# Performance work log

Hardware: AMD Instinct MI355X
Metric: run time of the kernel (lower is better)

Reference implementation:

```python
import math
import jax, jax.numpy as jnp
import numpy as np

EMBED_DIM = 512
NUM_HEADS = 8
EDGE_VOC = 16
EDGE_PAD = 0
L, B = 512, 16


def setup_inputs() -> dict:
    key = jax.random.key(0)
    ks = jax.random.split(key, 8)
    x = jax.random.normal(ks[0], (L, B, EMBED_DIM), dtype=jnp.float32)
    edge = jax.random.randint(ks[1], (B, L, L), 0, EDGE_VOC, dtype=jnp.int32)
    key_padding_mask = jnp.zeros((B, L), dtype=bool)
    # causal additive mask, as from nn.Transformer.generate_square_subsequent_mask
    attn_mask = jnp.where(jnp.triu(jnp.ones((L, L), bool), k=1), -jnp.inf, 0.0).astype(jnp.float32)
    s = 1.0 / math.sqrt(EMBED_DIM)
    in_proj_w = jax.random.uniform(ks[2], (3 * EMBED_DIM, EMBED_DIM), jnp.float32, -s, s)
    in_proj_b = jnp.zeros((3 * EMBED_DIM,), jnp.float32)
    out_proj_w = jax.random.uniform(ks[3], (EMBED_DIM, EMBED_DIM), jnp.float32, -s, s)
    out_proj_b = jnp.zeros((EMBED_DIM,), jnp.float32)
    edge_emb = jax.random.normal(ks[4], (EDGE_VOC, NUM_HEADS), dtype=jnp.float32)
    edge_emb = edge_emb.at[EDGE_PAD].set(0.0)  # padding_idx row zeroed
    return {"x": x, "edge": edge, "key_padding_mask": key_padding_mask,
            "attn_mask": attn_mask, "in_proj_w": in_proj_w, "in_proj_b": in_proj_b,
            "out_proj_w": out_proj_w, "out_proj_b": out_proj_b, "edge_emb": edge_emb}


def reference(x, edge, key_padding_mask, attn_mask,
              in_proj_w, in_proj_b, out_proj_w, out_proj_b, edge_emb):
    length, bsz, embed_dim = x.shape
    H = edge_emb.shape[1]
    hd = embed_dim // H
    qkv = x @ in_proj_w.T + in_proj_b                       # (L, B, 3E)
    q, k, v = jnp.split(qkv, 3, axis=-1)
    # (L, B*H, hd) -> (B*H, L, hd)
    q = q.reshape(length, bsz * H, hd).transpose(1, 0, 2)
    k = k.reshape(length, bsz * H, hd).transpose(1, 0, 2)
    v = v.reshape(length, bsz * H, hd).transpose(1, 0, 2)
    # combine attn_mask with key padding
    mask = attn_mask[None]                                   # (1, L, L)
    kpm = jnp.broadcast_to(key_padding_mask[:, None, None, :],
                           (bsz, H, 1, length)).reshape(bsz * H, 1, length)
    mask = jnp.where(kpm, -jnp.inf, mask)                    # (B*H, 1/L, L)
    # edge bias: (B, L, L, H) -> (B*H, L, L)
    ebias = edge_emb[edge].transpose(0, 3, 1, 2).reshape(bsz * H, length, length)
    q = q / math.sqrt(hd)
    scores = jnp.einsum('bqd,bkd->bqk', q, k) + mask + ebias
    attn = jax.nn.softmax(scores, axis=-1)
    out = jnp.einsum('bqk,bkd->bqd', attn, v)                # (B*H, L, hd)
    out = out.transpose(1, 0, 2).reshape(length, bsz, embed_dim)
    return out @ out_proj_w.T + out_proj_b
```

## Files before the change

### kernel.cpp

```cpp
#include <hip/hip_runtime.h>
#include <hip/hip_bf16.h>


typedef __attribute__((ext_vector_type(8))) short bf16x8;
typedef __attribute__((ext_vector_type(4))) float f32x4;
typedef __attribute__((ext_vector_type(4))) int i32x4;

#define LOG2E 1.44269504088896340736f

__device__ inline void gll16(const void* g, const void* l) {
  __builtin_amdgcn_global_load_lds(
      (const __attribute__((address_space(1))) unsigned int*)g,
      (__attribute__((address_space(3))) unsigned int*)l, 16, 0, 0);
}

__device__ inline short f2bf(float x) {
  __hip_bfloat16 t = __float2bfloat16(x);
  return *reinterpret_cast<short*>(&t);
}

__device__ inline void cstore(__hip_bfloat16* C, size_t idx, float v) {
  C[idx] = __float2bfloat16(v);
}
__device__ inline void cstore(float* C, size_t idx, float v) { C[idx] = v; }

__global__ void cvt3(const float* __restrict__ x, const float* __restrict__ w1,
                     const float* __restrict__ w2, __hip_bfloat16* __restrict__ xb,
                     __hip_bfloat16* __restrict__ w1b,
                     __hip_bfloat16* __restrict__ w2b) {
  const int blk = blockIdx.x;
  const float* src;
  __hip_bfloat16* dst;
  int off;
  if (blk < 2048)      { src = x;  dst = xb;  off = blk; }
  else if (blk < 2432) { src = w1; dst = w1b; off = blk - 2048; }
  else                 { src = w2; dst = w2b; off = blk - 2432; }
  const int i = (off * 256 + threadIdx.x) * 8;
  const float4 a = *(const float4*)(src + i);
  const float4 b = *(const float4*)(src + i + 4);
  bf16x8 r;
  r[0] = f2bf(a.x); r[1] = f2bf(a.y); r[2] = f2bf(a.z); r[3] = f2bf(a.w);
  r[4] = f2bf(b.x); r[5] = f2bf(b.y); r[6] = f2bf(b.z); r[7] = f2bf(b.w);
  *(bf16x8*)(dst + i) = r;
}

template <int MT, int RB, typename TC>
__global__ __launch_bounds__(256, RB) void gemm_bt(
    const __hip_bfloat16* __restrict__ A,
    const __hip_bfloat16* __restrict__ W,
    const float* __restrict__ bias,
    TC* __restrict__ C, int N, int K) {
  constexpr int MI = MT / 32;
  __shared__ short As[MT * 32];
  __shared__ short Ws[128 * 32];
  const int tid = threadIdx.x;
  const int wave = tid >> 6, lane = tid & 63;
  const int c = lane & 15, quad = lane >> 4;
  const int nb = N >> 7;
  const int bx = blockIdx.x % nb, by = blockIdx.x / nb;
  const int m0 = by * MT, n0 = bx << 7;
  const int wm = wave >> 1, wn = wave & 1;

  f32x4 acc[MI][4] = {};
  const int ar = lane >> 2;
  const int ak = (lane & 3) * 8;

  for (int k0 = 0; k0 < K; k0 += 32) {
    __syncthreads();
#pragma unroll
    for (int i = 0; i < MT / 64; i++) {
      const int r0 = i * 64 + wave * 16;
      gll16(A + (size_t)(m0 + r0 + ar) * K + k0 + ak, &As[r0 * 32]);
    }
#pragma unroll
    for (int i = 0; i < 2; i++) {
      const int r0 = i * 64 + wave * 16;
      gll16(W + (size_t)(n0 + r0 + ar) * K + k0 + ak, &Ws[r0 * 32]);
    }
    __syncthreads();
    bf16x8 af[MI], bfr[4];
#pragma unroll
    for (int i = 0; i < MI; i++)
      af[i] = *(const bf16x8*)&As[(wm * (MT / 2) + i * 16 + c) * 32 + quad * 8];
#pragma unroll
    for (int j = 0; j < 4; j++)
      bfr[j] = *(const bf16x8*)&Ws[(wn * 64 + j * 16 + c) * 32 + quad * 8];
#pragma unroll
    for (int i = 0; i < MI; i++)
#pragma unroll
      for (int j = 0; j < 4; j++)
        acc[i][j] = __builtin_amdgcn_mfma_f32_16x16x32_bf16(af[i], bfr[j],
                                                            acc[i][j], 0, 0, 0);
  }
#pragma unroll
  for (int j = 0; j < 4; j++) {
    const int col = n0 + wn * 64 + j * 16 + c;
    const float bv = bias[col];
#pragma unroll
    for (int i = 0; i < MI; i++) {
      const int row = m0 + wm * (MT / 2) + i * 16 + quad * 4;
#pragma unroll
      for (int r = 0; r < 4; r++)
        cstore(C, (size_t)(row + r) * N + col, acc[i][j][r] + bv);
    }
  }
}

__global__ __launch_bounds__(256, 4) void attn_kernel(
    const __hip_bfloat16* __restrict__ qkv,
    const int* __restrict__ edge,
    const float* __restrict__ edge_emb,
    __hip_bfloat16* __restrict__ attn_out) {
  __shared__ short Ks[64 * 72];
  __shared__ short Vt[64 * 72];
  __shared__ short Ps[4][16 * 72];
  __shared__ float eeS[16];

  const int tid = threadIdx.x;
  const int wave = tid >> 6, lane = tid & 63;
  const int c = lane & 15, quad = lane >> 4;
  const int i = blockIdx.x;
  constexpr int pi[8] = {0, 7, 1, 6, 2, 5, 3, 4};
  const int xcd = i & 7;
  const int j = i >> 3;
  const int qb = pi[j & 7];
  const int h = (j >> 3) & 7;
  const int b = xcd + ((j >> 6) << 3);
  const int colq = h * 64;

  if (tid < 16) eeS[tid] = (edge_emb[tid * 8 + h] - 16.0f) * LOG2E;

  const int q_g = (qb << 6) + wave * 16 + c;
  bf16x8 qf0, qf1;
  {
    const __hip_bfloat16* qp_ = qkv + (size_t)(q_g * 16 + b) * 1536 + colq;
    qf0 = *(const bf16x8*)(qp_ + quad * 8);
    qf1 = *(const bf16x8*)(qp_ + 32 + quad * 8);
  }
  float lsum = 0.f;
  f32x4 o[4] = {};
  const int* erow = edge + ((size_t)(b * 512 + q_g)) * 512;

  const int r2 = tid >> 3;
  const int cc = (tid & 7) * 8;
  const int kcol0 = ((r2 << 1) & 7) | (((r2 >> 2) ^ (cc >> 3)) << 3);
  const size_t sbase0 = (size_t)((r2 * 2) * 16 + b) * 1536 + colq + cc;
  bf16x8 kreg[2], vreg[2];
  kreg[0] = *(const bf16x8*)(qkv + sbase0 + 512);
  vreg[0] = *(const bf16x8*)(qkv + sbase0 + 1024);
  kreg[1] = *(const bf16x8*)(qkv + sbase0 + 24576 + 512);
  vreg[1] = *(const bf16x8*)(qkv + sbase0 + 24576 + 1024);

  __syncthreads();

  const int nkt = qb + 1;
  for (int kt = 0; kt < nkt; kt++) {
    const int k0 = kt << 6;
    if (kt) __syncthreads();
    *(bf16x8*)&Ks[(r2 * 2) * 72 + cc] = kreg[0];
    *(bf16x8*)&Ks[(r2 * 2 + 1) * 72 + cc] = kreg[1];
#pragma unroll
    for (int j2 = 0; j2 < 8; j2++) {
      short2 p;
      p.x = vreg[0][j2];
      p.y = vreg[1][j2];
      *(short2*)&Vt[(cc + j2) * 72 + kcol0] = p;
    }
    if (kt + 1 < nkt) {
      const size_t nb_ = sbase0 + (size_t)(kt + 1) * 64 * 24576;
      kreg[0] = *(const bf16x8*)(qkv + nb_ + 512);
      vreg[0] = *(const bf16x8*)(qkv + nb_ + 1024);
      kreg[1] = *(const bf16x8*)(qkv + nb_ + 24576 + 512);
      vreg[1] = *(const bf16x8*)(qkv + nb_ + 24576 + 1024);
    }
    i32x4 e4[4];
#pragma unroll
    for (int mt = 0; mt < 4; mt++)
      e4[mt] = *(const i32x4*)(erow + k0 + mt * 16 + quad * 4);
    __syncthreads();

    f32x4 st[4];
#pragma unroll
    for (int mt = 0; mt < 4; mt++) {
      const bf16x8 ka = *(const bf16x8*)&Ks[(mt * 16 + c) * 72 + quad * 8];
      const bf16x8 kb = *(const bf16x8*)&Ks[(mt * 16 + c) * 72 + 32 + quad * 8];
      f32x4 z = {0.f, 0.f, 0.f, 0.f};
      z = __builtin_amdgcn_mfma_f32_16x16x32_bf16(ka, qf0, z, 0, 0, 0);
      st[mt] = __builtin_amdgcn_mfma_f32_16x16x32_bf16(kb, qf1, z, 0, 0, 0);
    }
    float rsum = 0.0f;
#pragma unroll
    for (int mt = 0; mt < 4; mt++) {
      short4 pk;
#pragma unroll
      for (int r = 0; r < 4; r++) {
        const int key = k0 + mt * 16 + quad * 4 + r;
        const float p = (key <= q_g)
            ? exp2f(fmaf(st[mt][r], 0.125f * LOG2E, eeS[e4[mt][r] & 15]))
            : 0.0f;
        rsum += p;
        ((short*)&pk)[r] = f2bf(p);
      }
      *(short4*)&Ps[wave][c * 72 + mt * 16 + quad * 4] = pk;
    }
    lsum += rsum;
    const bf16x8 pa0 = *(const bf16x8*)&Ps[wave][c * 72 + quad * 8];
    const bf16x8 pa1 = *(const bf16x8*)&Ps[wave][c * 72 + 32 + quad * 8];
#pragma unroll
    for (int nt = 0; nt < 4; nt++) {
      const int n = nt * 16 + c;
      const bf16x8 vb0 = *(const bf16x8*)&Vt[n * 72 + ((quad ^ (n >> 3)) << 3)];
      const bf16x8 vb1 =
          *(const bf16x8*)&Vt[n * 72 + (((4 + quad) ^ (n >> 3)) << 3)];
      o[nt] = __builtin_amdgcn_mfma_f32_16x16x32_bf16(pa0, vb0, o[nt], 0, 0, 0);
      o[nt] = __builtin_amdgcn_mfma_f32_16x16x32_bf16(pa1, vb1, o[nt], 0, 0, 0);
    }
  }

  float l = lsum;
  l += __shfl_xor(l, 16);
  l += __shfl_xor(l, 32);
  float lr[4];
#pragma unroll
  for (int r = 0; r < 4; r++) lr[r] = __shfl(l, quad * 4 + r, 16);
  const int qrow0 = (qb << 6) + wave * 16 + quad * 4;
#pragma unroll
  for (int nt = 0; nt < 4; nt++)
#pragma unroll
    for (int r = 0; r < 4; r++)
      attn_out[(size_t)((qrow0 + r) * 16 + b) * 512 + colq + nt * 16 + c] =
          __float2bfloat16(o[nt][r] / lr[r]);
}

extern "C" void kernel_launch(void* const* d_in, const int* in_sizes, int n_in,
                              void* d_out, int out_size, void* d_ws, size_t ws_size,
                              hipStream_t stream) {
  const float* x    = (const float*)d_in[0];
  const int* edge   = (const int*)d_in[1];
  const float* ipw  = (const float*)d_in[4];
  const float* ipb  = (const float*)d_in[5];
  const float* opw  = (const float*)d_in[6];
  const float* opb  = (const float*)d_in[7];
  const float* eemb = (const float*)d_in[8];
  float* out = (float*)d_out;

  __hip_bfloat16* qkv  = (__hip_bfloat16*)d_ws;
  __hip_bfloat16* attn = qkv + (size_t)8192 * 1536;
  __hip_bfloat16* xb   = attn + (size_t)8192 * 512;
  __hip_bfloat16* w1b  = xb + (size_t)8192 * 512;
  __hip_bfloat16* w2b  = w1b + (size_t)1536 * 512;

  cvt3<<<2560, 256, 0, stream>>>(x, ipw, opw, xb, w1b, w2b);
  gemm_bt<128, 3, __hip_bfloat16>
      <<<768, 256, 0, stream>>>(xb, w1b, ipb, qkv, 1536, 512);
  attn_kernel<<<1024, 256, 0, stream>>>(qkv, edge, eemb, attn);
  gemm_bt<64, 2, float>
      <<<512, 256, 0, stream>>>(attn, w2b, opb, out, 512, 512);
}
```

Measured before the change: 155.6 us.

## Skip masked causal tiles on diagonal, fold QK scale into projection, seed MFMA with bias

On the diagonal key tile, each wave now computes only the 16-key sub-tiles at or below its query rows and skips the upper half of the PV MFMAs when they are all masked. The softmax scale times log2e is folded into the Q columns of the QKV projection epilogue. The edge bias is loaded as the MFMA accumulator seed, which removes the per-element fma. s_setprio hints are placed around the MFMA sections. Together these cut wasted causal work and VALU instructions in the attention inner loop, at the cost of more branches and storing Q pre-scaled in bf16, which changes rounding slightly. The bias lookup also relies on eeS being pre-scaled by log2e in code not shown, and the edge & 15 guard is dropped.

```diff
diff --git a/kernel.cpp b/kernel.cpp
--- a/kernel.cpp
+++ b/kernel.cpp
@@ -7,6 +7,7 @@
 typedef __attribute__((ext_vector_type(4))) int i32x4;
 
 #define LOG2E 1.44269504088896340736f
+#define QK_SCALE 0.18033688011112042f
 
 __device__ inline void gll16(const void* g, const void* l) {
   __builtin_amdgcn_global_load_lds(
@@ -44,7 +45,7 @@
   *(bf16x8*)(dst + i) = r;
 }
 
-template <int MT, int RB, typename TC>
+template <int MT, int RB, typename TC, bool QS = false>
 __global__ __launch_bounds__(256, RB) void gemm_bt(
     const __hip_bfloat16* __restrict__ A,
     const __hip_bfloat16* __restrict__ W,
@@ -100,8 +101,13 @@
     for (int i = 0; i < MI; i++) {
       const int row = m0 + wm * (MT / 2) + i * 16 + quad * 4;
 #pragma unroll
-      for (int r = 0; r < 4; r++)
-        cstore(C, (size_t)(row + r) * N + col, acc[i][j][r] + bv);
+      for (int r = 0; r < 4; r++) {
+        float v = acc[i][j][r] + bv;
+        if constexpr (QS) {
+          if (col < 512) v *= QK_SCALE;
+        }
+        cstore(C, (size_t)(row + r) * N + col, v);
+      }
     }
   }
 }
@@ -156,6 +162,8 @@
   const int nkt = qb + 1;
   for (int kt = 0; kt < nkt; kt++) {
     const int k0 = kt << 6;
+    const bool last = (kt == qb);
+    const int mtmax = last ? (wave + 1) : 4;
     if (kt) __syncthreads();
     *(bf16x8*)&Ks[(r2 * 2) * 72 + cc] = kreg[0];
     *(bf16x8*)&Ks[(r2 * 2 + 1) * 72 + cc] = kreg[1];
@@ -176,45 +184,67 @@
     i32x4 e4[4];
 #pragma unroll
     for (int mt = 0; mt < 4; mt++)
-      e4[mt] = *(const i32x4*)(erow + k0 + mt * 16 + quad * 4);
+      if (mt < mtmax)
+        e4[mt] = *(const i32x4*)(erow + k0 + mt * 16 + quad * 4);
     __syncthreads();
 
     f32x4 st[4];
+    __builtin_amdgcn_s_setprio(1);
 #pragma unroll
     for (int mt = 0; mt < 4; mt++) {
+      if (mt >= mtmax) continue;
+      f32x4 z;
+#pragma unroll
+      for (int r = 0; r < 4; r++) z[r] = eeS[e4[mt][r]];
       const bf16x8 ka = *(const bf16x8*)&Ks[(mt * 16 + c) * 72 + quad * 8];
       const bf16x8 kb = *(const bf16x8*)&Ks[(mt * 16 + c) * 72 + 32 + quad * 8];
-      f32x4 z = {0.f, 0.f, 0.f, 0.f};
       z = __builtin_amdgcn_mfma_f32_16x16x32_bf16(ka, qf0, z, 0, 0, 0);
       st[mt] = __builtin_amdgcn_mfma_f32_16x16x32_bf16(kb, qf1, z, 0, 0, 0);
     }
-    float rsum = 0.0f;
+    __builtin_amdgcn_s_setprio(0);
+
+    float rs[4] = {0.f, 0.f, 0.f, 0.f};
 #pragma unroll
     for (int mt = 0; mt < 4; mt++) {
-      short4 pk;
-#pragma unroll
-      for (int r = 0; r < 4; r++) {
-        const int key = k0 + mt * 16 + quad * 4 + r;
-        const float p = (key <= q_g)
-            ? exp2f(fmaf(st[mt][r], 0.125f * LOG2E, eeS[e4[mt][r] & 15]))
-            : 0.0f;
-        rsum += p;
-        ((short*)&pk)[r] = f2bf(p);
+      short4 pk = {0, 0, 0, 0};
+      if (mt < mtmax) {
+        if (last && mt == wave) {
+#pragma unroll
+          for (int r = 0; r < 4; r++) {
+            const float p = (quad * 4 + r <= c) ? exp2f(st[mt][r]) : 0.0f;
+            rs[r] += p;
+            ((short*)&pk)[r] = f2bf(p);
+          }
+        } else {
+#pragma unroll
+          for (int r = 0; r < 4; r++) {
+            const float p = exp2f(st[mt][r]);
+            rs[r] += p;
+            ((short*)&pk)[r] = f2bf(p);
+          }
+        }
       }
       *(short4*)&Ps[wave][c * 72 + mt * 16 + quad * 4] = pk;
     }
-    lsum += rsum;
+    lsum += (rs[0] + rs[1]) + (rs[2] + rs[3]);
+
+    const bool skip_hi = last && (wave < 2);
     const bf16x8 pa0 = *(const bf16x8*)&Ps[wave][c * 72 + quad * 8];
-    const bf16x8 pa1 = *(const bf16x8*)&Ps[wave][c * 72 + 32 + quad * 8];
+    bf16x8 pa1;
+    if (!skip_hi) pa1 = *(const bf16x8*)&Ps[wave][c * 72 + 32 + quad * 8];
+    __builtin_amdgcn_s_setprio(1);
 #pragma unroll
     for (int nt = 0; nt < 4; nt++) {
       const int n = nt * 16 + c;
       const bf16x8 vb0 = *(const bf16x8*)&Vt[n * 72 + ((quad ^ (n >> 3)) << 3)];
-      const bf16x8 vb1 =
-          *(const bf16x8*)&Vt[n * 72 + (((4 + quad) ^ (n >> 3)) << 3)];
       o[nt] = __builtin_amdgcn_mfma_f32_16x16x32_bf16(pa0, vb0, o[nt], 0, 0, 0);
-      o[nt] = __builtin_amdgcn_mfma_f32_16x16x32_bf16(pa1, vb1, o[nt], 0, 0, 0);
-    }
+      if (!skip_hi) {
+        const bf16x8 vb1 =
+            *(const bf16x8*)&Vt[n * 72 + (((4 + quad) ^ (n >> 3)) << 3)];
+        o[nt] = __builtin_amdgcn_mfma_f32_16x16x32_bf16(pa1, vb1, o[nt], 0, 0, 0);
+      }
+    }
+    __builtin_amdgcn_s_setprio(0);
   }
 
   float l = lsum;
@@ -251,7 +281,7 @@
   __hip_bfloat16* w2b  = w1b + (size_t)1536 * 512;
 
   cvt3<<<2560, 256, 0, stream>>>(x, ipw, opw, xb, w1b, w2b);
-  gemm_bt<128, 3, __hip_bfloat16>
+  gemm_bt<128, 3, __hip_bfloat16, true>
       <<<768, 256, 0, stream>>>(xb, w1b, ipb, qkv, 1536, 512);
   attn_kernel<<<1024, 256, 0, stream>>>(qkv, edge, eemb, attn);
   gemm_bt<64, 2, float>
```

After: 152.0 us. 1.02x faster.
